# Kernel tuning notes

Hardware: AMD Instinct MI355X
Metric: run time of the kernel (lower is better)

## Reference

```python
import jax, jax.numpy as jnp
import numpy as np

B, T, D = 2, 1024, 2048
E, K, H = 64, 4, 512          # n_experts, top-k, expert_dim
S, HS = 2, H * K              # shared experts, shared hidden dim
CAP = 512


def setup_inputs() -> dict:
    key = jax.random.key(0)
    ks = jax.random.split(key, 9)
    scale = 0.02
    return {
        "x": jax.random.normal(ks[0], (B, T, D), jnp.float32),
        "Wr": jax.random.normal(ks[1], (D, E), jnp.float32) * scale,
        "router_bias": jnp.zeros((E,), jnp.float32),
        "Wg": jax.random.normal(ks[2], (E, D, H), jnp.float32) * scale,
        "Wu": jax.random.normal(ks[3], (E, D, H), jnp.float32) * scale,
        "Wd": jax.random.normal(ks[4], (E, H, D), jnp.float32) * scale,
        "Sg": jax.random.normal(ks[5], (S, D, HS), jnp.float32) * scale,
        "Su": jax.random.normal(ks[6], (S, D, HS), jnp.float32) * scale,
        "Sd": jax.random.normal(ks[7], (S, HS, D), jnp.float32) * scale,
    }


def reference(x, Wr, router_bias, Wg, Wu, Wd, Sg, Su, Sd):
    Bx, Tx, Dx = x.shape
    N = Bx * Tx
    flat = x.reshape(N, Dx)                              # [N, D]

    # ---- router ----
    logits = flat @ Wr + router_bias                     # [N, E]
    scores = jax.nn.softmax(logits, axis=-1)
    topk_scores, topk_idx = jax.lax.top_k(scores, K)     # [N, K]
    topk_scores = topk_scores / topk_scores.sum(-1, keepdims=True)

    eid = topk_idx.reshape(-1)                           # [N*K] expert per assignment
    w = topk_scores.reshape(-1)                          # [N*K] combine weight
    tok = jnp.repeat(jnp.arange(N), K)                   # [N*K] source token id

    # position of each assignment within its expert's buffer
    oh = jax.nn.one_hot(eid, E, dtype=jnp.int32)         # [N*K, E]
    pos = ((jnp.cumsum(oh, axis=0) * oh).sum(-1) - 1)    # [N*K]
    valid = pos < CAP

    # ---- dispatch: scatter tokens into per-expert buffers ----
    xb = jnp.zeros((E, CAP, Dx), x.dtype).at[eid, pos].set(flat[tok], mode="drop")

    # ---- grouped SwiGLU expert FFN ----
    h = jax.nn.silu(jnp.einsum("ecd,edh->ech", xb, Wg)) * jnp.einsum("ecd,edh->ech", xb, Wu)
    yb = jnp.einsum("ech,ehd->ecd", h, Wd)               # [E, CAP, D]

    # ---- combine: gather back and weighted scatter-add to tokens ----
    y = yb[eid, jnp.minimum(pos, CAP - 1)] * (w * valid)[:, None]
    out = jnp.zeros((N, Dx), x.dtype).at[tok].add(y)

    # ---- always-on shared experts ----
    hs = jax.nn.silu(jnp.einsum("nd,sdh->nsh", flat, Sg)) * jnp.einsum("nd,sdh->nsh", flat, Su)
    out = out + jnp.einsum("nsh,shd->nd", hs, Sd)

    return out.reshape(Bx, Tx, Dx)
```

## Files before the change

kernel.cpp:

```cpp
#include <hip/hip_runtime.h>
#include <hip/hip_bf16.h>
#include <stdint.h>

#define N_TOK 2048
#define DM    2048
#define NEXP  64
#define TOPK  4
#define HEXP  512
#define CAPC  512
#define NSH   2
#define HSH   2048
#define RTB   8

typedef __attribute__((ext_vector_type(8))) short short8;
typedef __attribute__((ext_vector_type(4))) float f32x4;
typedef __attribute__((ext_vector_type(4))) float f4;

#define GLDS16(g, l) __builtin_amdgcn_global_load_lds(                     \
    (const __attribute__((address_space(1))) void*)(g),                    \
    (__attribute__((address_space(3))) void*)(l), 16, 0, 0)

static __device__ __forceinline__ unsigned short f2bf(float f) {
  union { float f; unsigned u; } v; v.f = f;
  unsigned r = v.u + 0x7FFFu + ((v.u >> 16) & 1u);
  return (unsigned short)(r >> 16);
}

__global__ __launch_bounds__(256) void k_convert(const float* __restrict__ x,
                                                 unsigned short* __restrict__ xb) {
  int i = (blockIdx.x * 256 + threadIdx.x) * 8;
  f4 a = *(const f4*)(x + i);
  f4 b = *(const f4*)(x + i + 4);
  short8 o;
  o[0]=f2bf(a[0]); o[1]=f2bf(a[1]); o[2]=f2bf(a[2]); o[3]=f2bf(a[3]);
  o[4]=f2bf(b[0]); o[5]=f2bf(b[1]); o[6]=f2bf(b[2]); o[7]=f2bf(b[3]);
  *(short8*)(xb + i) = o;
}

#define ARGMAX_ROUND(S,I)                                            \
  { float bv = v; int bi = lane;                                     \
    _Pragma("unroll")                                                \
    for (int o = 32; o; o >>= 1) {                                   \
      float ov = __shfl_xor(bv, o); int oi = __shfl_xor(bi, o);      \
      if (ov > bv || (ov == bv && oi < bi)) { bv = ov; bi = oi; }    \
    }                                                                \
    S = bv; I = bi; if (lane == bi) v = -1.f; }

__global__ __launch_bounds__(256) void k_router(const float* __restrict__ x,
    const float* __restrict__ Wr, const float* __restrict__ bias,
    int* __restrict__ cnt, int* __restrict__ lists, float* __restrict__ wlist) {
  __shared__ float part[4][RTB][64];
  __shared__ float logits[RTB][64];
  int t = threadIdx.x;
  int e = t & 63, sl = t >> 6;
  int tok0 = blockIdx.x * RTB;
  const float* xp = x + (size_t)tok0 * DM;
  float acc[RTB];
#pragma unroll
  for (int i = 0; i < RTB; ++i) acc[i] = 0.f;
  for (int d = sl * 512; d < sl * 512 + 512; ++d) {
    float w = Wr[(size_t)d * NEXP + e];
#pragma unroll
    for (int i = 0; i < RTB; ++i) acc[i] += xp[(size_t)i * DM + d] * w;
  }
#pragma unroll
  for (int i = 0; i < RTB; ++i) part[sl][i][e] = acc[i];
  __syncthreads();
  for (int i = sl; i < RTB; i += 4)
    logits[i][e] = part[0][i][e] + part[1][i][e] + part[2][i][e] + part[3][i][e] + bias[e];
  __syncthreads();
  int lane = t & 63, wv = t >> 6;
  for (int i = wv * 2; i < wv * 2 + 2; ++i) {
    float lg = logits[i][lane];
    float m = lg;
#pragma unroll
    for (int o = 32; o; o >>= 1) m = fmaxf(m, __shfl_xor(m, o));
    float p = expf(lg - m);
    float sm = p;
#pragma unroll
    for (int o = 32; o; o >>= 1) sm += __shfl_xor(sm, o);
    float v = p / sm;
    float s0, s1, s2, s3; int i0, i1, i2, i3;
    ARGMAX_ROUND(s0, i0)
    ARGMAX_ROUND(s1, i1)
    ARGMAX_ROUND(s2, i2)
    ARGMAX_ROUND(s3, i3)
    float tot = s0 + s1 + s2 + s3;
    if (lane < TOPK) {
      float myw = (lane == 0 ? s0 : lane == 1 ? s1 : lane == 2 ? s2 : s3) / tot;
      int   mye = (lane == 0 ? i0 : lane == 1 ? i1 : lane == 2 ? i2 : i3);
      int pos = atomicAdd(&cnt[mye], 1);
      if (pos < CAPC) {
        lists[mye * CAPC + pos] = tok0 + i;
        wlist[mye * CAPC + pos] = myw;
      }
    }
  }
}

__global__ void k_offs(const int* __restrict__ cnt, int* __restrict__ offs) {
  int l = threadIdx.x;
  int c = min(cnt[l], CAPC);
  int sum = c;
#pragma unroll
  for (int o = 1; o < 64; o <<= 1) {
    int ov = __shfl_up(sum, o);
    if (l >= o) sum += ov;
  }
  offs[l + 1] = sum;
  if (l == 0) offs[0] = 0;
}


static __device__ __forceinline__ short8 frag_ldA(const unsigned short* lds, int row, int kElem) {
  int byte = row * 128 + kElem * 2;
  byte ^= (row & 7) << 4;
  return *(const short8*)((const char*)lds + byte);
}

static __device__ __forceinline__ short8 bfragB(const float* lB, int nl, int kb) {
  short8 r;
#pragma unroll
  for (int j = 0; j < 8; ++j) r[j] = (short)f2bf(lB[(kb + j) * 64 + nl]);
  return r;
}

static __device__ __forceinline__ void mma1f(const unsigned short* lA, const float* lB,
    f32x4 (&acc)[4][2], int wm, int wn, int lane) {
  int r16 = lane & 15;
  int kg  = (lane >> 4) * 8;
#pragma unroll
  for (int kk = 0; kk < 2; ++kk) {
    int kb = kk * 32 + kg;
    short8 a[4], b[2];
#pragma unroll
    for (int mf = 0; mf < 4; ++mf) a[mf] = frag_ldA(lA, wm + mf * 16 + r16, kb);
#pragma unroll
    for (int nf = 0; nf < 2; ++nf) b[nf] = bfragB(lB, wn + nf * 16 + r16, kb);
#pragma unroll
    for (int mf = 0; mf < 4; ++mf)
#pragma unroll
      for (int nf = 0; nf < 2; ++nf)
        acc[mf][nf] = __builtin_amdgcn_mfma_f32_16x16x32_bf16(a[mf], b[nf], acc[mf][nf], 0, 0, 0);
  }
}

static __device__ __forceinline__ void mma2f(const unsigned short* lA,
    const float* lBg, const float* lBu,
    f32x4 (&accg)[4][2], f32x4 (&accu)[4][2], int wm, int wn, int lane) {
  int r16 = lane & 15;
  int kg  = (lane >> 4) * 8;
#pragma unroll
  for (int kk = 0; kk < 2; ++kk) {
    int kb = kk * 32 + kg;
    short8 a[4], bg[2], bu[2];
#pragma unroll
    for (int mf = 0; mf < 4; ++mf) a[mf] = frag_ldA(lA, wm + mf * 16 + r16, kb);
#pragma unroll
    for (int nf = 0; nf < 2; ++nf) {
      bg[nf] = bfragB(lBg, wn + nf * 16 + r16, kb);
      bu[nf] = bfragB(lBu, wn + nf * 16 + r16, kb);
    }
#pragma unroll
    for (int mf = 0; mf < 4; ++mf)
#pragma unroll
      for (int nf = 0; nf < 2; ++nf) {
        accg[mf][nf] = __builtin_amdgcn_mfma_f32_16x16x32_bf16(a[mf], bg[nf], accg[mf][nf], 0, 0, 0);
        accu[mf][nf] = __builtin_amdgcn_mfma_f32_16x16x32_bf16(a[mf], bu[nf], accu[mf][nf], 0, 0, 0);
      }
  }
}

static __device__ __forceinline__ float silu_mul(float g, float u) {
  return g / (1.f + expf(-g)) * u;
}

#define A_SETUP(asrc, SROW_EXPR)                                            \
  const unsigned short* asrc[4];                                            \
  {                                                                         \
    _Pragma("unroll")                                                       \
    for (int p = 0; p < 4; ++p) {                                           \
      int row = wv * 32 + p * 8 + (lane >> 3);                              \
      int srow = (SROW_EXPR);                                               \
      asrc[p] = Abase + (size_t)srow * lda + (((lane & 7) ^ (row & 7)) << 3);\
    }                                                                       \
  }

#define B_SETUP(bsrc, Bbase, ldb)                                           \
  const float* bsrc[4];                                                     \
  {                                                                         \
    _Pragma("unroll")                                                       \
    for (int p = 0; p < 4; ++p) {                                           \
      int k = wv * 16 + p * 4 + (lane >> 4);                                \
      bsrc[p] = (Bbase) + (size_t)k * (ldb) + n0 + (lane & 15) * 4;         \
    }                                                                       \
  }

#define A_STAGE(asrc, lA, k0)                                               \
  _Pragma("unroll")                                                         \
  for (int p = 0; p < 4; ++p) GLDS16(asrc[p] + (k0), (lA) + wv * 2048 + p * 512);

#define B_STAGE(bsrc, lB, k0, ldb)                                          \
  _Pragma("unroll")                                                         \
  for (int p = 0; p < 4; ++p) GLDS16(bsrc[p] + (size_t)(k0) * (ldb), (lB) + wv * 1024 + p * 256);

__global__ __launch_bounds__(256, 3) void k_expert_gateup(const unsigned short* __restrict__ xbf,
    const float* __restrict__ Wg, const float* __restrict__ Wu,
    const int* __restrict__ cnt, const int* __restrict__ offs,
    const int* __restrict__ lists, unsigned short* __restrict__ hws) {
  int e = blockIdx.y;
  int ne = min(cnt[e], CAPC);
  if (ne == 0) return;
  int n0 = blockIdx.x * 64;
  const float* Bg = Wg + (size_t)e * DM * HEXP;
  const float* Bu = Wu + (size_t)e * DM * HEXP;
  const int* lst = lists + e * CAPC;
  int base = offs[e];
  __shared__ unsigned short lA[128 * 64];
  __shared__ float lBg[64 * 64];
  __shared__ float lBu[64 * 64];
  int tid = threadIdx.x;
  int lane = tid & 63, wv = tid >> 6;
  int wm = (wv >> 1) * 64, wn = (wv & 1) * 32;
  const unsigned short* Abase = xbf; const int lda = DM;
  B_SETUP(bgsrc, Bg, HEXP)
  B_SETUP(busrc, Bu, HEXP)
  for (int m0 = 0; m0 < ne; m0 += 128) {
    A_SETUP(asrc, lst[min(m0 + row, ne - 1)])
    f32x4 accg[4][2] = {};
    f32x4 accu[4][2] = {};
    for (int k0 = 0; k0 < DM; k0 += 64) {
      A_STAGE(asrc, lA, k0)
      B_STAGE(bgsrc, lBg, k0, HEXP)
      B_STAGE(busrc, lBu, k0, HEXP)
      __syncthreads();
      mma2f(lA, lBg, lBu, accg, accu, wm, wn, lane);
      __syncthreads();
    }
#pragma unroll
    for (int mf = 0; mf < 4; ++mf)
#pragma unroll
      for (int r = 0; r < 4; ++r) {
        int rl = m0 + wm + mf * 16 + (lane >> 4) * 4 + r;
        if (rl < ne) {
#pragma unroll
          for (int nf = 0; nf < 2; ++nf) {
            int col = n0 + wn + nf * 16 + (lane & 15);
            float h = silu_mul(accg[mf][nf][r], accu[mf][nf][r]);
            hws[(size_t)(base + rl) * HEXP + col] = f2bf(h);
          }
        }
      }
  }
}

__global__ __launch_bounds__(256, 3) void k_shared_gateup(const unsigned short* __restrict__ xbf,
    const float* __restrict__ Sg, const float* __restrict__ Su,
    unsigned short* __restrict__ hs) {
  int n0 = blockIdx.x * 64;
  int m0 = blockIdx.y * 128;
  int s  = blockIdx.z;
  const float* Bg = Sg + (size_t)s * DM * HSH;
  const float* Bu = Su + (size_t)s * DM * HSH;
  __shared__ unsigned short lA[128 * 64];
  __shared__ float lBg[64 * 64];
  __shared__ float lBu[64 * 64];
  int tid = threadIdx.x;
  int lane = tid & 63, wv = tid >> 6;
  int wm = (wv >> 1) * 64, wn = (wv & 1) * 32;
  const unsigned short* Abase = xbf; const int lda = DM;
  B_SETUP(bgsrc, Bg, HSH)
  B_SETUP(busrc, Bu, HSH)
  A_SETUP(asrc, m0 + row)
  f32x4 accg[4][2] = {};
  f32x4 accu[4][2] = {};
  for (int k0 = 0; k0 < DM; k0 += 64) {
    A_STAGE(asrc, lA, k0)
    B_STAGE(bgsrc, lBg, k0, HSH)
    B_STAGE(busrc, lBu, k0, HSH)
    __syncthreads();
    mma2f(lA, lBg, lBu, accg, accu, wm, wn, lane);
    __syncthreads();
  }
#pragma unroll
  for (int mf = 0; mf < 4; ++mf)
#pragma unroll
    for (int nf = 0; nf < 2; ++nf)
#pragma unroll
      for (int r = 0; r < 4; ++r) {
        int row = m0 + wm + mf * 16 + (lane >> 4) * 4 + r;
        int col = n0 + wn + nf * 16 + (lane & 15);
        float h = silu_mul(accg[mf][nf][r], accu[mf][nf][r]);
        hs[(size_t)row * (NSH * HSH) + s * HSH + col] = f2bf(h);
      }
}

__global__ __launch_bounds__(256, 3) void k_shared_down(const unsigned short* __restrict__ hs,
    const float* __restrict__ Sd, float* __restrict__ out) {
  int n0 = blockIdx.x * 64;
  int m0 = blockIdx.y * 128;
  __shared__ unsigned short lA[128 * 64];
  __shared__ float lB[64 * 64];
  int tid = threadIdx.x;
  int lane = tid & 63, wv = tid >> 6;
  int wm = (wv >> 1) * 64, wn = (wv & 1) * 32;
  const unsigned short* Abase = hs; const int lda = NSH * HSH;
  B_SETUP(bsrc, Sd, DM)
  A_SETUP(asrc, m0 + row)
  f32x4 acc[4][2] = {};
  for (int k0 = 0; k0 < NSH * HSH; k0 += 64) {
    A_STAGE(asrc, lA, k0)
    B_STAGE(bsrc, lB, k0, DM)
    __syncthreads();
    mma1f(lA, lB, acc, wm, wn, lane);
    __syncthreads();
  }
#pragma unroll
  for (int mf = 0; mf < 4; ++mf)
#pragma unroll
    for (int nf = 0; nf < 2; ++nf)
#pragma unroll
      for (int r = 0; r < 4; ++r) {
        int row = m0 + wm + mf * 16 + (lane >> 4) * 4 + r;
        int col = n0 + wn + nf * 16 + (lane & 15);
        out[(size_t)row * DM + col] = acc[mf][nf][r];
      }
}

__global__ __launch_bounds__(256, 3) void k_expert_down(const unsigned short* __restrict__ hws,
    const float* __restrict__ Wd, const int* __restrict__ cnt, const int* __restrict__ offs,
    const int* __restrict__ lists, const float* __restrict__ wlist,
    float* __restrict__ out) {
  int e = blockIdx.y;
  int ne = min(cnt[e], CAPC);
  if (ne == 0) return;
  int n0 = blockIdx.x * 64;
  const float* B = Wd + (size_t)e * HEXP * DM;
  __shared__ unsigned short lA[128 * 64];
  __shared__ float lB[64 * 64];
  int tid = threadIdx.x;
  int lane = tid & 63, wv = tid >> 6;
  int wm = (wv >> 1) * 64, wn = (wv & 1) * 32;
  const unsigned short* Abase = hws + (size_t)offs[e] * HEXP; const int lda = HEXP;
  B_SETUP(bsrc, B, DM)
  for (int m0 = 0; m0 < ne; m0 += 128) {
    A_SETUP(asrc, min(m0 + row, ne - 1))
    f32x4 acc[4][2] = {};
    for (int k0 = 0; k0 < HEXP; k0 += 64) {
      A_STAGE(asrc, lA, k0)
      B_STAGE(bsrc, lB, k0, DM)
      __syncthreads();
      mma1f(lA, lB, acc, wm, wn, lane);
      __syncthreads();
    }
#pragma unroll
    for (int mf = 0; mf < 4; ++mf)
#pragma unroll
      for (int r = 0; r < 4; ++r) {
        int rl = m0 + wm + mf * 16 + (lane >> 4) * 4 + r;
        if (rl < ne) {
          int tok  = lists[e * CAPC + rl];
          float w  = wlist[e * CAPC + rl];
#pragma unroll
          for (int nf = 0; nf < 2; ++nf) {
            int col = n0 + wn + nf * 16 + (lane & 15);
            atomicAdd(out + (size_t)tok * DM + col, acc[mf][nf][r] * w);
          }
        }
      }
  }
}

extern "C" void kernel_launch(void* const* d_in, const int* in_sizes, int n_in,
                              void* d_out, int out_size, void* d_ws, size_t ws_size,
                              hipStream_t stream) {
  const float* x    = (const float*)d_in[0];
  const float* Wr   = (const float*)d_in[1];
  const float* bias = (const float*)d_in[2];
  const float* Wg   = (const float*)d_in[3];
  const float* Wu   = (const float*)d_in[4];
  const float* Wd   = (const float*)d_in[5];
  const float* Sg   = (const float*)d_in[6];
  const float* Su   = (const float*)d_in[7];
  const float* Sd   = (const float*)d_in[8];
  float* out = (float*)d_out;
  char* ws = (char*)d_ws;

  const size_t off_cnt   = 0;
  const size_t off_offs  = 256;
  const size_t off_lists = 1024;
  const size_t off_wlist = off_lists + (size_t)NEXP * CAPC * 4;
  const size_t off_xbf   = off_wlist + (size_t)NEXP * CAPC * 4;
  const size_t off_hs    = off_xbf + (size_t)N_TOK * DM * 2;
  const size_t off_h     = off_hs + (size_t)N_TOK * NSH * HSH * 2;
  const size_t req       = off_h + (size_t)N_TOK * TOPK * HEXP * 2;
  if (ws_size < req) return;

  int* cnt            = (int*)(ws + off_cnt);
  int* offs           = (int*)(ws + off_offs);
  int* lists          = (int*)(ws + off_lists);
  float* wlist        = (float*)(ws + off_wlist);
  unsigned short* xbf = (unsigned short*)(ws + off_xbf);
  unsigned short* hs  = (unsigned short*)(ws + off_hs);
  unsigned short* hws = (unsigned short*)(ws + off_h);

  hipMemsetAsync(cnt, 0, NEXP * sizeof(int), stream);
  k_convert<<<(N_TOK * DM) / (256 * 8), 256, 0, stream>>>(x, xbf);
  k_router<<<N_TOK / RTB, 256, 0, stream>>>(x, Wr, bias, cnt, lists, wlist);
  k_offs<<<1, 64, 0, stream>>>(cnt, offs);
  k_expert_gateup<<<dim3(HEXP / 64, NEXP), 256, 0, stream>>>(xbf, Wg, Wu, cnt, offs, lists, hws);
  k_shared_gateup<<<dim3(HSH / 64, N_TOK / 128, NSH), 256, 0, stream>>>(xbf, Sg, Su, hs);
  k_shared_down<<<dim3(DM / 64, N_TOK / 128), 256, 0, stream>>>(hs, Sd, out);
  k_expert_down<<<dim3(DM / 64, NEXP), 256, 0, stream>>>(hws, Wd, cnt, offs, lists, wlist, out);
}
```

Measured before the change: 670.9 us.

## Pipeline GEMMs with 4-stage LDS buffers and split gate/up into separate passes

Every GEMM kernel now uses a 4-deep ring of K=32 LDS stages with async global-to-LDS loads and explicit vmcnt waits and barriers, replacing the load-sync-compute-sync loop. Gate and up projections are split into separate blocks that store bf16 intermediates, followed by standalone SwiGLU elementwise kernels. Other changes: new LDS swizzles, packed bf16 conversion via v_cvt_pk_bf16_f32, a remapped 1D grid with expert interleaving, and launch bounds lowered to 2 blocks per SM. The cost is extra global traffic for the intermediates, two more launches, and bf16 rounding of gate/up before the SiLU.

```diff
diff --git a/kernel.cpp b/kernel.cpp
--- a/kernel.cpp
+++ b/kernel.cpp
@@ -15,15 +15,27 @@
 typedef __attribute__((ext_vector_type(8))) short short8;
 typedef __attribute__((ext_vector_type(4))) float f32x4;
 typedef __attribute__((ext_vector_type(4))) float f4;
+typedef __attribute__((ext_vector_type(4))) unsigned uint4v;
 
 #define GLDS16(g, l) __builtin_amdgcn_global_load_lds(                     \
     (const __attribute__((address_space(1))) void*)(g),                    \
     (__attribute__((address_space(3))) void*)(l), 16, 0, 0)
+
+#define VMWAIT(N) asm volatile("s_waitcnt vmcnt(" #N ")" ::: "memory")
+#define BARX() do { asm volatile("" ::: "memory");                          \
+                    __builtin_amdgcn_s_barrier();                           \
+                    asm volatile("" ::: "memory"); } while (0)
 
 static __device__ __forceinline__ unsigned short f2bf(float f) {
   union { float f; unsigned u; } v; v.f = f;
   unsigned r = v.u + 0x7FFFu + ((v.u >> 16) & 1u);
   return (unsigned short)(r >> 16);
+}
+
+static __device__ __forceinline__ unsigned pk2(float lo, float hi) {
+  unsigned u;
+  asm("v_cvt_pk_bf16_f32 %0, %1, %2" : "=v"(u) : "v"(lo), "v"(hi));
+  return u;
 }
 
 __global__ __launch_bounds__(256) void k_convert(const float* __restrict__ x,
@@ -111,64 +123,34 @@
   if (l == 0) offs[0] = 0;
 }
 
-
 static __device__ __forceinline__ short8 frag_ldA(const unsigned short* lds, int row, int kElem) {
-  int byte = row * 128 + kElem * 2;
-  byte ^= (row & 7) << 4;
+  int byte = row * 64 + kElem * 2;
+  byte ^= ((row >> 1) & 3) << 4;
   return *(const short8*)((const char*)lds + byte);
 }
 
 static __device__ __forceinline__ short8 bfragB(const float* lB, int nl, int kb) {
-  short8 r;
-#pragma unroll
-  for (int j = 0; j < 8; ++j) r[j] = (short)f2bf(lB[(kb + j) * 64 + nl]);
-  return r;
+  const float* p = lB + kb * 64 + (nl ^ (((kb >> 3) & 1) << 4));
+  float f0 = p[0],   f1 = p[64],  f2 = p[128], f3 = p[192];
+  float f4_ = p[256], f5 = p[320], f6 = p[384], f7 = p[448];
+  uint4v uv = { pk2(f0, f1), pk2(f2, f3), pk2(f4_, f5), pk2(f6, f7) };
+  return __builtin_bit_cast(short8, uv);
 }
 
 static __device__ __forceinline__ void mma1f(const unsigned short* lA, const float* lB,
     f32x4 (&acc)[4][2], int wm, int wn, int lane) {
   int r16 = lane & 15;
-  int kg  = (lane >> 4) * 8;
-#pragma unroll
-  for (int kk = 0; kk < 2; ++kk) {
-    int kb = kk * 32 + kg;
-    short8 a[4], b[2];
-#pragma unroll
-    for (int mf = 0; mf < 4; ++mf) a[mf] = frag_ldA(lA, wm + mf * 16 + r16, kb);
-#pragma unroll
-    for (int nf = 0; nf < 2; ++nf) b[nf] = bfragB(lB, wn + nf * 16 + r16, kb);
-#pragma unroll
-    for (int mf = 0; mf < 4; ++mf)
-#pragma unroll
-      for (int nf = 0; nf < 2; ++nf)
-        acc[mf][nf] = __builtin_amdgcn_mfma_f32_16x16x32_bf16(a[mf], b[nf], acc[mf][nf], 0, 0, 0);
-  }
-}
-
-static __device__ __forceinline__ void mma2f(const unsigned short* lA,
-    const float* lBg, const float* lBu,
-    f32x4 (&accg)[4][2], f32x4 (&accu)[4][2], int wm, int wn, int lane) {
-  int r16 = lane & 15;
-  int kg  = (lane >> 4) * 8;
-#pragma unroll
-  for (int kk = 0; kk < 2; ++kk) {
-    int kb = kk * 32 + kg;
-    short8 a[4], bg[2], bu[2];
-#pragma unroll
-    for (int mf = 0; mf < 4; ++mf) a[mf] = frag_ldA(lA, wm + mf * 16 + r16, kb);
-#pragma unroll
-    for (int nf = 0; nf < 2; ++nf) {
-      bg[nf] = bfragB(lBg, wn + nf * 16 + r16, kb);
-      bu[nf] = bfragB(lBu, wn + nf * 16 + r16, kb);
-    }
-#pragma unroll
-    for (int mf = 0; mf < 4; ++mf)
-#pragma unroll
-      for (int nf = 0; nf < 2; ++nf) {
-        accg[mf][nf] = __builtin_amdgcn_mfma_f32_16x16x32_bf16(a[mf], bg[nf], accg[mf][nf], 0, 0, 0);
-        accu[mf][nf] = __builtin_amdgcn_mfma_f32_16x16x32_bf16(a[mf], bu[nf], accu[mf][nf], 0, 0, 0);
-      }
-  }
+  int kb  = (lane >> 4) * 8;
+  short8 a[4], b[2];
+#pragma unroll
+  for (int mf = 0; mf < 4; ++mf) a[mf] = frag_ldA(lA, wm + mf * 16 + r16, kb);
+#pragma unroll
+  for (int nf = 0; nf < 2; ++nf) b[nf] = bfragB(lB, wn + nf * 16 + r16, kb);
+#pragma unroll
+  for (int mf = 0; mf < 4; ++mf)
+#pragma unroll
+    for (int nf = 0; nf < 2; ++nf)
+      acc[mf][nf] = __builtin_amdgcn_mfma_f32_16x16x32_bf16(a[mf], b[nf], acc[mf][nf], 0, 0, 0);
 }
 
 static __device__ __forceinline__ float silu_mul(float g, float u) {
@@ -176,67 +158,87 @@
 }
 
 #define A_SETUP(asrc, SROW_EXPR)                                            \
-  const unsigned short* asrc[4];                                            \
+  const unsigned short* asrc[2];                                            \
   {                                                                         \
     _Pragma("unroll")                                                       \
-    for (int p = 0; p < 4; ++p) {                                           \
-      int row = wv * 32 + p * 8 + (lane >> 3);                              \
+    for (int p = 0; p < 2; ++p) {                                           \
+      int row = p * 64 + wv * 16 + (lane >> 2);                             \
       int srow = (SROW_EXPR);                                               \
-      asrc[p] = Abase + (size_t)srow * lda + (((lane & 7) ^ (row & 7)) << 3);\
+      asrc[p] = Abase + (size_t)srow * lda                                  \
+              + (((lane & 3) ^ ((row >> 1) & 3)) << 3);                     \
     }                                                                       \
   }
+#define A_STAGE(asrc, lAbuf, k0)                                            \
+  { _Pragma("unroll")                                                       \
+    for (int p = 0; p < 2; ++p)                                             \
+      GLDS16(asrc[p] + (k0), (lAbuf) + p * 2048 + wv * 512); }
 
 #define B_SETUP(bsrc, Bbase, ldb)                                           \
-  const float* bsrc[4];                                                     \
+  const float* bsrc[2];                                                     \
   {                                                                         \
     _Pragma("unroll")                                                       \
-    for (int p = 0; p < 4; ++p) {                                           \
-      int k = wv * 16 + p * 4 + (lane >> 4);                                \
-      bsrc[p] = (Bbase) + (size_t)k * (ldb) + n0 + (lane & 15) * 4;         \
+    for (int p = 0; p < 2; ++p) {                                           \
+      int k = p * 16 + wv * 4 + (lane >> 4);                                \
+      int c = (lane & 15) ^ (((k >> 3) & 1) << 2);                          \
+      bsrc[p] = (Bbase) + (size_t)k * (ldb) + n0 + c * 4;                   \
     }                                                                       \
   }
-
-#define A_STAGE(asrc, lA, k0)                                               \
-  _Pragma("unroll")                                                         \
-  for (int p = 0; p < 4; ++p) GLDS16(asrc[p] + (k0), (lA) + wv * 2048 + p * 512);
-
-#define B_STAGE(bsrc, lB, k0, ldb)                                          \
-  _Pragma("unroll")                                                         \
-  for (int p = 0; p < 4; ++p) GLDS16(bsrc[p] + (size_t)(k0) * (ldb), (lB) + wv * 1024 + p * 256);
-
-__global__ __launch_bounds__(256, 3) void k_expert_gateup(const unsigned short* __restrict__ xbf,
+#define B_STAGE(bsrc, lBbuf, k0, ldb)                                       \
+  { _Pragma("unroll")                                                       \
+    for (int p = 0; p < 2; ++p)                                             \
+      GLDS16(bsrc[p] + (size_t)(k0) * (ldb), (lBbuf) + p * 1024 + wv * 256); }
+
+#define MM_STEP(q, tn, LDB)                                                 \
+  VMWAIT(12); BARX();                                                       \
+  mma1f(lA[q], lB[q], acc, wm, wn, lane);                                   \
+  BARX();                                                                   \
+  A_STAGE(asrc, lA[q], (tn) * 32)                                           \
+  B_STAGE(bsrc, lB[q], (tn) * 32, LDB)
+
+#define MM_PEEL(q, W)                                                       \
+  VMWAIT(W); BARX();                                                        \
+  mma1f(lA[q], lB[q], acc, wm, wn, lane);
+
+__global__ __launch_bounds__(256, 2) void k_mmE(const unsigned short* __restrict__ xbf,
     const float* __restrict__ Wg, const float* __restrict__ Wu,
     const int* __restrict__ cnt, const int* __restrict__ offs,
-    const int* __restrict__ lists, unsigned short* __restrict__ hws) {
-  int e = blockIdx.y;
+    const int* __restrict__ lists, unsigned short* __restrict__ hg,
+    unsigned short* __restrict__ hu) {
+  int bid = blockIdx.x;
+  int e   = ((bid & 7) << 3) | ((bid >> 3) & 7);
+  int nb  = (bid >> 6) & 7;
+  int mat = bid >> 9;
+  int n0 = nb * 64;
   int ne = min(cnt[e], CAPC);
   if (ne == 0) return;
-  int n0 = blockIdx.x * 64;
-  const float* Bg = Wg + (size_t)e * DM * HEXP;
-  const float* Bu = Wu + (size_t)e * DM * HEXP;
+  const float* B = (mat ? Wu : Wg) + (size_t)e * DM * HEXP;
+  unsigned short* hdst = mat ? hu : hg;
   const int* lst = lists + e * CAPC;
   int base = offs[e];
-  __shared__ unsigned short lA[128 * 64];
-  __shared__ float lBg[64 * 64];
-  __shared__ float lBu[64 * 64];
-  int tid = threadIdx.x;
-  int lane = tid & 63, wv = tid >> 6;
+  __shared__ unsigned short lA[4][128 * 32];
+  __shared__ float lB[4][32 * 64];
+  int tid = threadIdx.x, lane = tid & 63, wv = tid >> 6;
   int wm = (wv >> 1) * 64, wn = (wv & 1) * 32;
   const unsigned short* Abase = xbf; const int lda = DM;
-  B_SETUP(bgsrc, Bg, HEXP)
-  B_SETUP(busrc, Bu, HEXP)
+  B_SETUP(bsrc, B, HEXP)
+  const int NT = DM / 32;
   for (int m0 = 0; m0 < ne; m0 += 128) {
     A_SETUP(asrc, lst[min(m0 + row, ne - 1)])
-    f32x4 accg[4][2] = {};
-    f32x4 accu[4][2] = {};
-    for (int k0 = 0; k0 < DM; k0 += 64) {
-      A_STAGE(asrc, lA, k0)
-      B_STAGE(bgsrc, lBg, k0, HEXP)
-      B_STAGE(busrc, lBu, k0, HEXP)
-      __syncthreads();
-      mma2f(lA, lBg, lBu, accg, accu, wm, wn, lane);
-      __syncthreads();
+    f32x4 acc[4][2] = {};
+#pragma unroll
+    for (int q = 0; q < 4; ++q) {
+      A_STAGE(asrc, lA[q], q * 32)
+      B_STAGE(bsrc, lB[q], q * 32, HEXP)
     }
+#pragma unroll 1
+    for (int t = 0; t < NT - 4; t += 4) {
+      MM_STEP(0, t + 4, HEXP)
+      MM_STEP(1, t + 5, HEXP)
+      MM_STEP(2, t + 6, HEXP)
+      MM_STEP(3, t + 7, HEXP)
+    }
+    MM_PEEL(0, 12) MM_PEEL(1, 8) MM_PEEL(2, 4) MM_PEEL(3, 0)
+    BARX();
 #pragma unroll
     for (int mf = 0; mf < 4; ++mf)
 #pragma unroll
@@ -246,42 +248,65 @@
 #pragma unroll
           for (int nf = 0; nf < 2; ++nf) {
             int col = n0 + wn + nf * 16 + (lane & 15);
-            float h = silu_mul(accg[mf][nf][r], accu[mf][nf][r]);
-            hws[(size_t)(base + rl) * HEXP + col] = f2bf(h);
+            hdst[(size_t)(base + rl) * HEXP + col] = f2bf(acc[mf][nf][r]);
           }
         }
       }
   }
 }
 
-__global__ __launch_bounds__(256, 3) void k_shared_gateup(const unsigned short* __restrict__ xbf,
+__global__ __launch_bounds__(256) void k_swiglu_e(const unsigned short* __restrict__ hg,
+    const unsigned short* __restrict__ hu, const int* __restrict__ offs,
+    unsigned short* __restrict__ hws) {
+  int total = offs[NEXP];
+  int gid = blockIdx.x * 256 + threadIdx.x;
+  int row = gid >> 6;
+  if (row >= total) return;
+  int c0 = (gid & 63) * 8;
+  size_t o = (size_t)row * HEXP + c0;
+  short8 g8 = *(const short8*)(hg + o);
+  short8 u8 = *(const short8*)(hu + o);
+  short8 r;
+#pragma unroll
+  for (int j = 0; j < 8; ++j) {
+    union { unsigned u; float f; } gg, uu;
+    gg.u = ((unsigned)(unsigned short)g8[j]) << 16;
+    uu.u = ((unsigned)(unsigned short)u8[j]) << 16;
+    r[j] = f2bf(silu_mul(gg.f, uu.f));
+  }
+  *(short8*)(hws + o) = r;
+}
+
+__global__ __launch_bounds__(256, 2) void k_mmS(const unsigned short* __restrict__ xbf,
     const float* __restrict__ Sg, const float* __restrict__ Su,
-    unsigned short* __restrict__ hs) {
-  int n0 = blockIdx.x * 64;
-  int m0 = blockIdx.y * 128;
-  int s  = blockIdx.z;
-  const float* Bg = Sg + (size_t)s * DM * HSH;
-  const float* Bu = Su + (size_t)s * DM * HSH;
-  __shared__ unsigned short lA[128 * 64];
-  __shared__ float lBg[64 * 64];
-  __shared__ float lBu[64 * 64];
-  int tid = threadIdx.x;
-  int lane = tid & 63, wv = tid >> 6;
+    unsigned short* __restrict__ hsg, unsigned short* __restrict__ hsu) {
+  int bid = blockIdx.x;
+  int nb = bid & 31, mb = (bid >> 5) & 15, s = (bid >> 9) & 1, mat = bid >> 10;
+  int n0 = nb * 64, m0 = mb * 128;
+  const float* B = (mat ? Su : Sg) + (size_t)s * DM * HSH;
+  unsigned short* hdst = mat ? hsu : hsg;
+  __shared__ unsigned short lA[4][128 * 32];
+  __shared__ float lB[4][32 * 64];
+  int tid = threadIdx.x, lane = tid & 63, wv = tid >> 6;
   int wm = (wv >> 1) * 64, wn = (wv & 1) * 32;
   const unsigned short* Abase = xbf; const int lda = DM;
-  B_SETUP(bgsrc, Bg, HSH)
-  B_SETUP(busrc, Bu, HSH)
+  B_SETUP(bsrc, B, HSH)
   A_SETUP(asrc, m0 + row)
-  f32x4 accg[4][2] = {};
-  f32x4 accu[4][2] = {};
-  for (int k0 = 0; k0 < DM; k0 += 64) {
-    A_STAGE(asrc, lA, k0)
-    B_STAGE(bgsrc, lBg, k0, HSH)
-    B_STAGE(busrc, lBu, k0, HSH)
-    __syncthreads();
-    mma2f(lA, lBg, lBu, accg, accu, wm, wn, lane);
-    __syncthreads();
-  }
+  f32x4 acc[4][2] = {};
+  const int NT = DM / 32;
+#pragma unroll
+  for (int q = 0; q < 4; ++q) {
+    A_STAGE(asrc, lA[q], q * 32)
+    B_STAGE(bsrc, lB[q], q * 32, HSH)
+  }
+#pragma unroll 1
+  for (int t = 0; t < NT - 4; t += 4) {
+    MM_STEP(0, t + 4, HSH)
+    MM_STEP(1, t + 5, HSH)
+    MM_STEP(2, t + 6, HSH)
+    MM_STEP(3, t + 7, HSH)
+  }
+  MM_PEEL(0, 12) MM_PEEL(1, 8) MM_PEEL(2, 4) MM_PEEL(3, 0)
 #pragma unroll
   for (int mf = 0; mf < 4; ++mf)
 #pragma unroll
@@ -290,31 +315,54 @@
       for (int r = 0; r < 4; ++r) {
         int row = m0 + wm + mf * 16 + (lane >> 4) * 4 + r;
         int col = n0 + wn + nf * 16 + (lane & 15);
-        float h = silu_mul(accg[mf][nf][r], accu[mf][nf][r]);
-        hs[(size_t)row * (NSH * HSH) + s * HSH + col] = f2bf(h);
+        hdst[(size_t)row * (NSH * HSH) + s * HSH + col] = f2bf(acc[mf][nf][r]);
       }
 }
 
-__global__ __launch_bounds__(256, 3) void k_shared_down(const unsigned short* __restrict__ hs,
+__global__ __launch_bounds__(256) void k_swiglu_s(const unsigned short* __restrict__ hsg,
+    const unsigned short* __restrict__ hsu, unsigned short* __restrict__ hs) {
+  int gid = blockIdx.x * 256 + threadIdx.x;
+  size_t o = (size_t)gid * 8;
+  short8 g8 = *(const short8*)(hsg + o);
+  short8 u8 = *(const short8*)(hsu + o);
+  short8 r;
+#pragma unroll
+  for (int j = 0; j < 8; ++j) {
+    union { unsigned u; float f; } gg, uu;
+    gg.u = ((unsigned)(unsigned short)g8[j]) << 16;
+    uu.u = ((unsigned)(unsigned short)u8[j]) << 16;
+    r[j] = f2bf(silu_mul(gg.f, uu.f));
+  }
+  *(short8*)(hs + o) = r;
+}
+
+__global__ __launch_bounds__(256, 2) void k_sd4(const unsigned short* __restrict__ hs,
     const float* __restrict__ Sd, float* __restrict__ out) {
-  int n0 = blockIdx.x * 64;
-  int m0 = blockIdx.y * 128;
-  __shared__ unsigned short lA[128 * 64];
-  __shared__ float lB[64 * 64];
-  int tid = threadIdx.x;
-  int lane = tid & 63, wv = tid >> 6;
+  int bid = blockIdx.x;
+  int nb = bid & 31, mb = bid >> 5;
+  int n0 = nb * 64, m0 = mb * 128;
+  __shared__ unsigned short lA[4][128 * 32];
+  __shared__ float lB[4][32 * 64];
+  int tid = threadIdx.x, lane = tid & 63, wv = tid >> 6;
   int wm = (wv >> 1) * 64, wn = (wv & 1) * 32;
   const unsigned short* Abase = hs; const int lda = NSH * HSH;
   B_SETUP(bsrc, Sd, DM)
   A_SETUP(asrc, m0 + row)
   f32x4 acc[4][2] = {};
-  for (int k0 = 0; k0 < NSH * HSH; k0 += 64) {
-    A_STAGE(asrc, lA, k0)
-    B_STAGE(bsrc, lB, k0, DM)
-    __syncthreads();
-    mma1f(lA, lB, acc, wm, wn, lane);
-    __syncthreads();
-  }
+  const int NT = (NSH * HSH) / 32;
+#pragma unroll
+  for (int q = 0; q < 4; ++q) {
+    A_STAGE(asrc, lA[q], q * 32)
+    B_STAGE(bsrc, lB[q], q * 32, DM)
+  }
+#pragma unroll 1
+  for (int t = 0; t < NT - 4; t += 4) {
+    MM_STEP(0, t + 4, DM)
+    MM_STEP(1, t + 5, DM)
+    MM_STEP(2, t + 6, DM)
+    MM_STEP(3, t + 7, DM)
+  }
+  MM_PEEL(0, 12) MM_PEEL(1, 8) MM_PEEL(2, 4) MM_PEEL(3, 0)
 #pragma unroll
   for (int mf = 0; mf < 4; ++mf)
 #pragma unroll
@@ -327,32 +375,41 @@
       }
 }
 
-__global__ __launch_bounds__(256, 3) void k_expert_down(const unsigned short* __restrict__ hws,
+__global__ __launch_bounds__(256, 2) void k_downE(const unsigned short* __restrict__ hws,
     const float* __restrict__ Wd, const int* __restrict__ cnt, const int* __restrict__ offs,
     const int* __restrict__ lists, const float* __restrict__ wlist,
     float* __restrict__ out) {
-  int e = blockIdx.y;
+  int bid = blockIdx.x;
+  int e  = ((bid & 7) << 3) | ((bid >> 3) & 7);
+  int nb = bid >> 6;
+  int n0 = nb * 64;
   int ne = min(cnt[e], CAPC);
   if (ne == 0) return;
-  int n0 = blockIdx.x * 64;
   const float* B = Wd + (size_t)e * HEXP * DM;
-  __shared__ unsigned short lA[128 * 64];
-  __shared__ float lB[64 * 64];
-  int tid = threadIdx.x;
-  int lane = tid & 63, wv = tid >> 6;
+  __shared__ unsigned short lA[4][128 * 32];
+  __shared__ float lB[4][32 * 64];
+  int tid = threadIdx.x, lane = tid & 63, wv = tid >> 6;
   int wm = (wv >> 1) * 64, wn = (wv & 1) * 32;
   const unsigned short* Abase = hws + (size_t)offs[e] * HEXP; const int lda = HEXP;
   B_SETUP(bsrc, B, DM)
+  const int NT = HEXP / 32;
   for (int m0 = 0; m0 < ne; m0 += 128) {
     A_SETUP(asrc, min(m0 + row, ne - 1))
     f32x4 acc[4][2] = {};
-    for (int k0 = 0; k0 < HEXP; k0 += 64) {
-      A_STAGE(asrc, lA, k0)
-      B_STAGE(bsrc, lB, k0, DM)
-      __syncthreads();
-      mma1f(lA, lB, acc, wm, wn, lane);
-      __syncthreads();
+#pragma unroll
+    for (int q = 0; q < 4; ++q) {
+      A_STAGE(asrc, lA[q], q * 32)
+      B_STAGE(bsrc, lB[q], q * 32, DM)
     }
+#pragma unroll 1
+    for (int t = 0; t < NT - 4; t += 4) {
+      MM_STEP(0, t + 4, DM)
+      MM_STEP(1, t + 5, DM)
+      MM_STEP(2, t + 6, DM)
+      MM_STEP(3, t + 7, DM)
+    }
+    MM_PEEL(0, 12) MM_PEEL(1, 8) MM_PEEL(2, 4) MM_PEEL(3, 0)
+    BARX();
 #pragma unroll
     for (int mf = 0; mf < 4; ++mf)
 #pragma unroll
@@ -392,8 +449,12 @@
   const size_t off_wlist = off_lists + (size_t)NEXP * CAPC * 4;
   const size_t off_xbf   = off_wlist + (size_t)NEXP * CAPC * 4;
   const size_t off_hs    = off_xbf + (size_t)N_TOK * DM * 2;
-  const size_t off_h     = off_hs + (size_t)N_TOK * NSH * HSH * 2;
-  const size_t req       = off_h + (size_t)N_TOK * TOPK * HEXP * 2;
+  const size_t off_hws   = off_hs + (size_t)N_TOK * NSH * HSH * 2;
+  const size_t off_hg    = off_hws + (size_t)N_TOK * TOPK * HEXP * 2;
+  const size_t off_hu    = off_hg + (size_t)N_TOK * TOPK * HEXP * 2;
+  const size_t off_hsg   = off_hu + (size_t)N_TOK * TOPK * HEXP * 2;
+  const size_t off_hsu   = off_hsg + (size_t)N_TOK * NSH * HSH * 2;
+  const size_t req       = off_hsu + (size_t)N_TOK * NSH * HSH * 2;
   if (ws_size < req) return;
 
   int* cnt            = (int*)(ws + off_cnt);
@@ -402,14 +463,23 @@
   float* wlist        = (float*)(ws + off_wlist);
   unsigned short* xbf = (unsigned short*)(ws + off_xbf);
   unsigned short* hs  = (unsigned short*)(ws + off_hs);
-  unsigned short* hws = (unsigned short*)(ws + off_h);
+  unsigned short* hws = (unsigned short*)(ws + off_hws);
+  unsigned short* hg  = (unsigned short*)(ws + off_hg);
+  unsigned short* hu  = (unsigned short*)(ws + off_hu);
+  unsigned short* hsg = (unsigned short*)(ws + off_hsg);
+  unsigned short* hsu = (unsigned short*)(ws + off_hsu);
 
   hipMemsetAsync(cnt, 0, NEXP * sizeof(int), stream);
   k_convert<<<(N_TOK * DM) / (256 * 8), 256, 0, stream>>>(x, xbf);
   k_router<<<N_TOK / RTB, 256, 0, stream>>>(x, Wr, bias, cnt, lists, wlist);
   k_offs<<<1, 64, 0, stream>>>(cnt, offs);
-  k_expert_gateup<<<dim3(HEXP / 64, NEXP), 256, 0, stream>>>(xbf, Wg, Wu, cnt, offs, lists, hws);
-  k_shared_gateup<<<dim3(HSH / 64, N_TOK / 128, NSH), 256, 0, stream>>>(xbf, Sg, Su, hs);
-  k_shared_down<<<dim3(DM / 64, N_TOK / 128), 256, 0, stream>>>(hs, Sd, out);
-  k_expert_down<<<dim3(DM / 64, NEXP), 256, 0, stream>>>(hws, Wd, cnt, offs, lists, wlist, out);
-}
+
+  k_mmE<<<1024, 256, 0, stream>>>(xbf, Wg, Wu, cnt, offs, lists, hg, hu);
+  k_swiglu_e<<<(N_TOK * TOPK * HEXP / 8) / 256, 256, 0, stream>>>(hg, hu, offs, hws);
+
+  k_mmS<<<2048, 256, 0, stream>>>(xbf, Sg, Su, hsg, hsu);
+  k_swiglu_s<<<(N_TOK * NSH * HSH / 8) / 256, 256, 0, stream>>>(hsg, hsu, hs);
+
+  k_sd4<<<512, 256, 0, stream>>>(hs, Sd, out);
+  k_downE<<<2048, 256, 0, stream>>>(hws, Wd, cnt, offs, lists, wlist, out);
+}
```

New measurement: 712.2 us. 1.06x slower.
